# Kernel tuning notes

Hardware: AMD Instinct MI355X
Metric: run time of the kernel (lower is better)

The kernel has to match this reference:

```python
import jax, jax.numpy as jnp
import numpy as np

TAU = 2.0
BN_EPS = 1e-5
SG_ALPHA = 4.0
ATTN_SCALE = 0.125
NUM_HEADS = 8
T, B, C, H, W = 2, 16, 256, 64, 64


@jax.custom_vjp
def heaviside(x):
    return (x >= 0.0).astype(x.dtype)

def _hv_fwd(x):
    return (x >= 0.0).astype(x.dtype), x

def _hv_bwd(x, g):
    s = jax.nn.sigmoid(SG_ALPHA * x)
    return (g * SG_ALPHA * s * (1.0 - s),)

heaviside.defvjp(_hv_fwd, _hv_bwd)


def lif(x_seq, v_th):
    # MultiStepLIFNode: v <- v + (x - v)/tau ; spike = H(v - v_th); hard reset to 0 (detached)
    def step(v, x):
        v = v + (x - v) / TAU
        s = heaviside(v - v_th)
        v = v * (1.0 - jax.lax.stop_gradient(s))
        return v, s
    _, spikes = jax.lax.scan(step, jnp.zeros_like(x_seq[0]), x_seq)
    return spikes


def bn1d(x, gamma, beta, mean, var):
    # eval-mode BatchNorm1d over channel axis 2 of [T,B,C,N]
    inv = (gamma / jnp.sqrt(var + BN_EPS)).reshape(1, 1, -1, 1)
    shift = (beta - mean * gamma / jnp.sqrt(var + BN_EPS)).reshape(1, 1, -1, 1)
    return x * inv + shift


def to_heads(t):
    # [T,B,C,N] -> [T,B,h,N,d]
    t_, b_, c_, n_ = t.shape
    d = c_ // NUM_HEADS
    return t.transpose(0, 1, 3, 2).reshape(t_, b_, n_, NUM_HEADS, d).transpose(0, 1, 3, 2, 4)


def setup_inputs() -> dict:
    key = jax.random.key(0)
    ks = jax.random.split(key, 24)
    w_scale = 0.06  # ~1/sqrt(C)
    inp = {
        'x': jax.random.normal(ks[0], (T, B, C, H, W), jnp.float32),
        'wq': jax.random.normal(ks[1], (C, C), jnp.float32) * w_scale,
        'wk': jax.random.normal(ks[2], (C, C), jnp.float32) * w_scale,
        'wv': jax.random.normal(ks[3], (C, C), jnp.float32) * w_scale,
        'wp': jax.random.normal(ks[4], (C, C), jnp.float32) * w_scale,
        'bp': jax.random.normal(ks[5], (C,), jnp.float32) * 0.1,
    }
    i = 6
    for p in ('q', 'k', 'v', 'p'):
        inp[p + '_gamma'] = jax.random.uniform(ks[i], (C,), jnp.float32, 0.5, 1.5); i += 1
        inp[p + '_beta'] = jax.random.normal(ks[i], (C,), jnp.float32) * 0.1; i += 1
        inp[p + '_mean'] = jax.random.normal(ks[i], (C,), jnp.float32) * 0.1; i += 1
        inp[p + '_var'] = jax.random.uniform(ks[i], (C,), jnp.float32, 0.5, 1.5); i += 1
    return inp


def reference(x, wq, wk, wv, wp, bp,
              q_gamma, q_beta, q_mean, q_var,
              k_gamma, k_beta, k_mean, k_var,
              v_gamma, v_beta, v_mean, v_var,
              p_gamma, p_beta, p_mean, p_var):
    t_, b_, c_, h_, w_ = x.shape
    n_ = h_ * w_
    xs = lif(x, 1.0).reshape(t_, b_, c_, n_)  # proj_lif then flatten(3)
    # 1x1 conv == channel matmul, then BN, then LIF (binary spikes)
    q_out = lif(bn1d(jnp.einsum('oc,tbcn->tbon', wq, xs), q_gamma, q_beta, q_mean, q_var), 1.0)
    k_out = lif(bn1d(jnp.einsum('oc,tbcn->tbon', wk, xs), k_gamma, k_beta, k_mean, k_var), 1.0)
    v_out = lif(bn1d(jnp.einsum('oc,tbcn->tbon', wv, xs), v_gamma, v_beta, v_mean, v_var), 1.0)
    q = to_heads(q_out)
    k = to_heads(k_out)
    v = to_heads(v_out)
    # linear attention: (k^T @ v) then q @ (k^T v)
    kv = jnp.einsum('tbhnd,tbhne->tbhde', k, v)  # [T,B,h,d,d]
    attn = jnp.einsum('tbhnd,tbhde->tbhne', q, kv) * ATTN_SCALE
    attn = attn.transpose(0, 1, 2, 4, 3).reshape(t_, b_, c_, n_)
    s = lif(attn, 0.5)  # attn_lif with v_threshold=0.5
    out = jnp.einsum('oc,tbcn->tbon', wp, s) + bp.reshape(1, 1, -1, 1)
    out = bn1d(out, p_gamma, p_beta, p_mean, p_var).reshape(t_, b_, c_, h_, w_)
    return (out, xs, q_out, k_out, v_out)
```

## Files before the change

kernel.cpp:

```cpp
#include <hip/hip_runtime.h>
#include <cstdint>
#include <cstddef>

typedef __attribute__((ext_vector_type(8))) short short8;
typedef __attribute__((ext_vector_type(4))) float floatx4;
typedef __attribute__((ext_vector_type(4))) unsigned int uintx4;

#define DEV static __device__ __forceinline__

constexpr int NT = 2, NB = 16, NC = 256, NN = 4096, NHD = 8;
constexpr size_t NE1 = (size_t)NT * NB * NC * NN;
constexpr size_t TSTRIDE = (size_t)NB * NC * NN;

DEV unsigned short f2bf(float x) {
  unsigned int u = __builtin_bit_cast(unsigned int, x);
  unsigned int lsb = (u >> 16) & 1u;
  u += 0x7FFFu + lsb;
  return (unsigned short)(u >> 16);
}
DEV float bfb2f(unsigned short h) {
  unsigned int u = ((unsigned int)h) << 16;
  return __builtin_bit_cast(float, u);
}
DEV unsigned int pk2(unsigned short a, unsigned short b) {
  return (unsigned int)a | ((unsigned int)b << 16);
}
DEV int swz(int fr, int kk) { return fr * 4 + (kk ^ ((fr >> 1) & 3)); }
typedef __attribute__((address_space(3))) unsigned int lds_u32;
typedef __attribute__((address_space(1))) const unsigned int glb_u32;
DEV void gld_lds16(const void* g, void* l) {
  __builtin_amdgcn_global_load_lds((glb_u32*)g, (lds_u32*)l, 16, 0, 0);
}

__global__ __launch_bounds__(256) void prep_kernel(
    const float* __restrict__ wq, const float* __restrict__ wk, const float* __restrict__ wv,
    const float* __restrict__ wp, const float* __restrict__ bp,
    const float* __restrict__ qg, const float* __restrict__ qb, const float* __restrict__ qm, const float* __restrict__ qva,
    const float* __restrict__ kg, const float* __restrict__ kb, const float* __restrict__ km, const float* __restrict__ kva,
    const float* __restrict__ vg, const float* __restrict__ vb, const float* __restrict__ vm, const float* __restrict__ vva,
    const float* __restrict__ pg, const float* __restrict__ pb, const float* __restrict__ pm, const float* __restrict__ pva,
    unsigned short* __restrict__ Wqkv, unsigned short* __restrict__ Wp,
    float* __restrict__ invqkv, float* __restrict__ shqkv,
    float* __restrict__ invp, float* __restrict__ shp)
{
  int idx = blockIdx.x * 256 + threadIdx.x;
  if (idx < 196608) {
    int o = idx >> 8, c = idx & 255;
    const float* src = (o < 256) ? wq : (o < 512) ? wk : wv;
    float w = src[(size_t)(o & 255) * 256 + c];
    unsigned short h0 = f2bf(w);  float f0 = bfb2f(h0);
    float r1 = w - f0;
    unsigned short h1 = f2bf(r1); float f1 = bfb2f(h1);
    float r2 = r1 - f1;
    unsigned short h2 = f2bf(r2);
    Wqkv[idx] = h0; Wqkv[196608 + idx] = h1; Wqkv[393216 + idx] = h2;
  } else if (idx < 262144) {
    int j = idx - 196608;
    float w = wp[j];
    unsigned short h0 = f2bf(w);  float f0 = bfb2f(h0);
    float r1 = w - f0;
    unsigned short h1 = f2bf(r1); float f1 = bfb2f(h1);
    float r2 = r1 - f1;
    unsigned short h2 = f2bf(r2);
    Wp[j] = h0; Wp[65536 + j] = h1; Wp[131072 + j] = h2;
  } else if (idx < 262912) {
    int i = idx - 262144;
    int p = i >> 8, c = i & 255;
    float g  = (p == 0) ? qg[c] : (p == 1) ? kg[c] : vg[c];
    float be = (p == 0) ? qb[c] : (p == 1) ? kb[c] : vb[c];
    float mn = (p == 0) ? qm[c] : (p == 1) ? km[c] : vm[c];
    float vr = (p == 0) ? qva[c] : (p == 1) ? kva[c] : vva[c];
    float sq = sqrtf(vr + 1e-5f);
    invqkv[i] = g / sq;
    shqkv[i]  = be - (mn * g) / sq;
  } else if (idx < 263168) {
    int c = idx - 262912;
    float sq = sqrtf(pva[c] + 1e-5f);
    float iv = pg[c] / sq;
    invp[c] = iv;
    shp[c]  = pb[c] - (pm[c] * pg[c]) / sq + bp[c] * iv;
  }
}

__global__ __launch_bounds__(256) void lifx_kernel(const float* __restrict__ x,
                                                   float* __restrict__ xs_out,
                                                   unsigned short* __restrict__ xb16)
{
  __shared__ float tile[2][64][65];
  const int nt = blockIdx.x, ct = blockIdx.y, b = blockIdx.z;
  const int tid = threadIdx.x;
  const int ci = tid >> 2, cq = tid & 3;
  const int n0 = nt * 64, c0 = ct * 64;
  const size_t rowbase = ((size_t)(b * NC + c0 + ci)) * NN + n0 + cq * 16;
  const float* px0 = x + rowbase;
  const float* px1 = x + rowbase + TSTRIDE;
  float* po0 = xs_out + rowbase;
  float* po1 = xs_out + rowbase + TSTRIDE;
  #pragma unroll
  for (int jj = 0; jj < 4; jj++) {
    floatx4 x0 = *(const floatx4*)(px0 + jj * 4);
    floatx4 x1 = *(const floatx4*)(px1 + jj * 4);
    floatx4 s0v, s1v;
    #pragma unroll
    for (int e = 0; e < 4; e++) {
      float v1 = x0[e] * 0.5f;
      float s0 = (v1 >= 1.0f) ? 1.0f : 0.0f;
      float vr = v1 * (1.0f - s0);
      float v2 = vr + (x1[e] - vr) * 0.5f;
      float s1 = (v2 >= 1.0f) ? 1.0f : 0.0f;
      s0v[e] = s0; s1v[e] = s1;
      tile[0][ci][cq * 16 + jj * 4 + e] = s0;
      tile[1][ci][cq * 16 + jj * 4 + e] = s1;
    }
    *(floatx4*)(po0 + jj * 4) = s0v;
    *(floatx4*)(po1 + jj * 4) = s1v;
  }
  __syncthreads();
  const int ni = tid >> 2, cg = tid & 3;
  #pragma unroll
  for (int t = 0; t < 2; t++) {
    unsigned int wbits = 0;
    #pragma unroll
    for (int j = 0; j < 16; j++)
      wbits |= (tile[t][cg * 16 + j][ni] != 0.f ? 1u : 0u) << j;
    xb16[((size_t)((t * NB + b) * NN) + n0 + ni) * 16 + (c0 >> 4) + cg] = (unsigned short)wbits;
  }
}

__global__ __launch_bounds__(256, 3) void qkv_gemm(
    const unsigned short* __restrict__ xb16,
    const unsigned short* __restrict__ Wsp,
    const float* __restrict__ invv, const float* __restrict__ shv,
    float* __restrict__ dq, float* __restrict__ dk, float* __restrict__ dv,
    unsigned short* __restrict__ qbits, unsigned short* __restrict__ kbits,
    unsigned short* __restrict__ vbits)
{
  __shared__ __align__(16) unsigned char smem[33280];
  unsigned short* Al = (unsigned short*)smem;
  unsigned short* Bl = (unsigned short*)(smem + 24576);
  float* yl = (float*)smem;
  const int nt = blockIdx.x, mt = blockIdx.y, b = blockIdx.z;
  const int tid = threadIdx.x;
  const int lane = tid & 63, quad = lane >> 4, l16 = lane & 15;
  const int wave = tid >> 6;
  const int tw = wave >> 1, wm = (wave & 1) * 64;
  floatx4 acc[4][4] = {};
  const int bt = tid >> 7, brow = (tid >> 1) & 63, bhalf = tid & 1;
  const unsigned short* xrow = xb16 + ((size_t)((bt * NB + b) * NN) + nt * 64 + brow) * 16 + bhalf;

  for (int k0 = 0; k0 < 256; k0 += 32) {
    __syncthreads();
    #pragma unroll
    for (int j = 0; j < 6; j++) {
      int ci = j * 256 + tid;
      int fr = ci >> 2;
      int kk = (ci & 3) ^ ((fr >> 1) & 3);
      int s = fr >> 7, row = fr & 127;
      const unsigned short* g = Wsp + (size_t)s * 196608 + (size_t)(mt * 128 + row) * 256 + k0 + kk * 8;
      gld_lds16(g, Al + (size_t)ci * 8);
    }
    {
      unsigned int wb = xrow[k0 >> 4];
      uintx4 c0v, c1v;
      #pragma unroll
      for (int p = 0; p < 4; p++) {
        c0v[p] = pk2(((wb >> (2 * p)) & 1) ? 0x3F80 : 0, ((wb >> (2 * p + 1)) & 1) ? 0x3F80 : 0);
        c1v[p] = pk2(((wb >> (8 + 2 * p)) & 1) ? 0x3F80 : 0, ((wb >> (9 + 2 * p)) & 1) ? 0x3F80 : 0);
      }
      int fr = bt * 64 + brow;
      *(uintx4*)(Bl + (size_t)swz(fr, bhalf * 2)     * 8) = c0v;
      *(uintx4*)(Bl + (size_t)swz(fr, bhalf * 2 + 1) * 8) = c1v;
    }
    __syncthreads();

    short8 bfr[4];
    #pragma unroll
    for (int ni = 0; ni < 4; ni++) {
      int fr = tw * 64 + ni * 16 + l16;
      bfr[ni] = *(const short8*)(Bl + (size_t)swz(fr, quad) * 8);
    }
    #pragma unroll
    for (int mi = 0; mi < 4; mi++) {
      const int r0 = wm + mi * 16 + l16;
      short8 a0 = *(const short8*)(Al + (size_t)swz(      r0, quad) * 8);
      short8 a1 = *(const short8*)(Al + (size_t)swz(128 + r0, quad) * 8);
      short8 a2 = *(const short8*)(Al + (size_t)swz(256 + r0, quad) * 8);
      #pragma unroll
      for (int ni = 0; ni < 4; ni++) {
        acc[mi][ni] = __builtin_amdgcn_mfma_f32_16x16x32_bf16(a0, bfr[ni], acc[mi][ni], 0, 0, 0);
        acc[mi][ni] = __builtin_amdgcn_mfma_f32_16x16x32_bf16(a1, bfr[ni], acc[mi][ni], 0, 0, 0);
        acc[mi][ni] = __builtin_amdgcn_mfma_f32_16x16x32_bf16(a2, bfr[ni], acc[mi][ni], 0, 0, 0);
      }
    }
  }
  __syncthreads();
  if (tw == 0) {
    #pragma unroll
    for (int mi = 0; mi < 4; mi++)
      #pragma unroll
      for (int r = 0; r < 4; r++)
        #pragma unroll
        for (int ni = 0; ni < 4; ni++)
          yl[(size_t)(wm + mi * 16 + quad * 4 + r) * 65 + ni * 16 + l16] = acc[mi][ni][r];
  }
  __syncthreads();
  if (tw == 1) {
    #pragma unroll
    for (int mi = 0; mi < 4; mi++) {
      #pragma unroll
      for (int r = 0; r < 4; r++) {
        const int lrow = wm + mi * 16 + quad * 4 + r;
        const int orow = mt * 128 + lrow;
        const float iv = invv[orow], sh = shv[orow];
        const int widx = orow >> 8, c = orow & 255;
        float* dst = (widx == 0) ? dq : (widx == 1) ? dk : dv;
        unsigned short* bb = (widx == 0) ? qbits : (widx == 1) ? kbits : vbits;
        #pragma unroll
        for (int ni = 0; ni < 4; ni++) {
          const int n = nt * 64 + ni * 16 + l16;
          float y0 = yl[(size_t)lrow * 65 + ni * 16 + l16] * iv + sh;
          float y1 = acc[mi][ni][r] * iv + sh;
          float v1 = y0 * 0.5f;
          float s0 = (v1 >= 1.0f) ? 1.0f : 0.0f;
          float vr = v1 * (1.0f - s0);
          float v2 = vr + (y1 - vr) * 0.5f;
          float s1 = (v2 >= 1.0f) ? 1.0f : 0.0f;
          dst[(size_t)(b * NC + c) * NN + n] = s0;
          dst[(size_t)((NB + b) * NC + c) * NN + n] = s1;
          unsigned long long bl0 = __ballot(s0 != 0.0f);
          unsigned long long bl1 = __ballot(s1 != 0.0f);
          if (l16 == 0) {
            const int w16 = nt * 4 + ni;
            bb[(size_t)b        * 65536 + (size_t)c * 256 + w16] = (unsigned short)(bl0 >> (quad * 16));
            bb[(size_t)(NB + b) * 65536 + (size_t)c * 256 + w16] = (unsigned short)(bl1 >> (quad * 16));
          }
        }
      }
    }
  }
}

__global__ __launch_bounds__(256) void kv_kernel(const unsigned long long* __restrict__ kb,
                                                 const unsigned long long* __restrict__ vb,
                                                 float* __restrict__ kvout)
{
  __shared__ unsigned long long Kl[32 * 65];
  __shared__ unsigned long long Vl[32 * 65];
  const int h = blockIdx.x, z = blockIdx.y;
  const int tid = threadIdx.x;
  for (int i = tid; i < 2048; i += 256) {
    int row = i >> 6, w = i & 63;
    size_t g = (size_t)z * 16384 + (size_t)(h * 32 + row) * 64 + w;
    Kl[row * 65 + w] = kb[g];
    Vl[row * 65 + w] = vb[g];
  }
  __syncthreads();
  const int d = tid & 31, e0 = tid >> 5;
  int acc0 = 0, acc1 = 0, acc2 = 0, acc3 = 0;
  for (int w = 0; w < 64; w++) {
    unsigned long long ku = Kl[d * 65 + w];
    acc0 += __popcll(ku & Vl[(e0     ) * 65 + w]);
    acc1 += __popcll(ku & Vl[(e0 +  8) * 65 + w]);
    acc2 += __popcll(ku & Vl[(e0 + 16) * 65 + w]);
    acc3 += __popcll(ku & Vl[(e0 + 24) * 65 + w]);
  }
  float* o = kvout + ((size_t)(z * NHD + h) << 10);
  o[d * 32 + e0     ] = (float)acc0;
  o[d * 32 + e0 +  8] = (float)acc1;
  o[d * 32 + e0 + 16] = (float)acc2;
  o[d * 32 + e0 + 24] = (float)acc3;
}

__global__ __launch_bounds__(256) void attn_kernel(const unsigned short* __restrict__ qb16,
                                                   const float* __restrict__ kvout,
                                                   unsigned short* __restrict__ sb16)
{
  __shared__ float kvl[2][32][33];
  __shared__ unsigned short qt[2][32][16];
  const int nb = blockIdx.x, h = blockIdx.y, b = blockIdx.z;
  const int tid = threadIdx.x;
  const int wave = tid >> 6, lane = tid & 63, quad = lane >> 4, l16 = lane & 15;
  for (int i = tid; i < 2048; i += 256) {
    int t = i >> 10, j = i & 1023;
    kvl[t][j >> 5][j & 31] = kvout[((size_t)((t * NB + b) * NHD + h) << 10) + j];
  }
  for (int i = tid; i < 1024; i += 256) {
    int t = i >> 9, j = i & 511, row = j >> 4, w = j & 15;
    qt[t][row][w] = qb16[(size_t)(t * NB + b) * 65536 + (size_t)(h * 32 + row) * 256 + nb * 16 + w];
  }
  __syncthreads();
  short8 bf[2][2][2];
  #pragma unroll
  for (int t = 0; t < 2; t++) {
    #pragma unroll
    for (int eh = 0; eh < 2; eh++) {
      short8 bh, bl;
      #pragma unroll
      for (int j = 0; j < 8; j++) {
        float v = kvl[t][quad * 8 + j][eh * 16 + l16];
        unsigned short h0 = f2bf(v);
        float lo = v - bfb2f(h0);
        bh[j] = (short)h0;
        bl[j] = (short)f2bf(lo);
      }
      bf[t][0][eh] = bh; bf[t][1][eh] = bl;
    }
  }
  floatx4 acc[2][4][2] = {};
  #pragma unroll
  for (int t = 0; t < 2; t++) {
    #pragma unroll
    for (int nt = 0; nt < 4; nt++) {
      const int wv = wave * 4 + nt;
      short8 af;
      #pragma unroll
      for (int j = 0; j < 8; j++) {
        unsigned short w = qt[t][quad * 8 + j][wv];
        af[j] = (short)(((w >> l16) & 1) ? 0x3F80 : 0);
      }
      #pragma unroll
      for (int eh = 0; eh < 2; eh++) {
        acc[t][nt][eh] = __builtin_amdgcn_mfma_f32_16x16x32_bf16(af, bf[t][0][eh], acc[t][nt][eh], 0, 0, 0);
        acc[t][nt][eh] = __builtin_amdgcn_mfma_f32_16x16x32_bf16(af, bf[t][1][eh], acc[t][nt][eh], 0, 0, 0);
      }
    }
  }
  const int n0 = nb * 256 + wave * 64;
  #pragma unroll
  for (int nt = 0; nt < 4; nt++) {
    #pragma unroll
    for (int r = 0; r < 4; r++) {
      const int n = n0 + nt * 16 + quad * 4 + r;
      #pragma unroll
      for (int eh = 0; eh < 2; eh++) {
        float a0 = acc[0][nt][eh][r] * 0.125f;
        float a1 = acc[1][nt][eh][r] * 0.125f;
        float v1 = a0 * 0.5f;
        float s0 = (v1 >= 0.5f) ? 1.f : 0.f;
        float vr = v1 * (1.f - s0);
        float v2 = vr + (a1 - vr) * 0.5f;
        float s1 = (v2 >= 0.5f) ? 1.f : 0.f;
        unsigned long long bl0 = __ballot(s0 != 0.f);
        unsigned long long bl1 = __ballot(s1 != 0.f);
        if (l16 == 0) {
          const int w16 = h * 2 + eh;
          sb16[(size_t)b        * 65536 + (size_t)n * 16 + w16] = (unsigned short)(bl0 >> (quad * 16));
          sb16[(size_t)(NB + b) * 65536 + (size_t)n * 16 + w16] = (unsigned short)(bl1 >> (quad * 16));
        }
      }
    }
  }
}

__global__ __launch_bounds__(256, 3) void p_gemm(
    const unsigned short* __restrict__ sb16,
    const unsigned short* __restrict__ Wsp,
    const float* __restrict__ invv, const float* __restrict__ shv,
    float* __restrict__ dout)
{
  __shared__ __align__(16) unsigned char smem[32768];
  unsigned short* Al = (unsigned short*)smem;
  unsigned short* Bl = (unsigned short*)(smem + 24576);
  const int nt = blockIdx.x, mt = blockIdx.y, z = blockIdx.z;
  const int tid = threadIdx.x;
  const int lane = tid & 63, quad = lane >> 4, l16 = lane & 15;
  const int wave = tid >> 6;
  const int wm = (wave & 1) * 64, wn = (wave >> 1) * 64;
  floatx4 acc[4][4] = {};
  const int brow = tid & 127, bhalf = tid >> 7;

  for (int k0 = 0; k0 < 256; k0 += 32) {
    __syncthreads();
    #pragma unroll
    for (int j = 0; j < 6; j++) {
      int ci = j * 256 + tid;
      int fr = ci >> 2;
      int kk = (ci & 3) ^ ((fr >> 1) & 3);
      int s = fr >> 7, row = fr & 127;
      const unsigned short* g = Wsp + (size_t)s * 65536 + (size_t)(mt * 128 + row) * 256 + k0 + kk * 8;
      gld_lds16(g, Al + (size_t)ci * 8);
    }
    {
      unsigned short wb = sb16[(size_t)z * 65536 + (size_t)(nt * 128 + brow) * 16 + (k0 >> 4) + bhalf];
      uintx4 lo4, hi4;
      #pragma unroll
      for (int p = 0; p < 4; p++) {
        lo4[p] = pk2(((wb >> (2 * p)) & 1) ? 0x3F80 : 0, ((wb >> (2 * p + 1)) & 1) ? 0x3F80 : 0);
        hi4[p] = pk2(((wb >> (8 + 2 * p)) & 1) ? 0x3F80 : 0, ((wb >> (9 + 2 * p)) & 1) ? 0x3F80 : 0);
      }
      *(uintx4*)(Bl + (size_t)swz(brow, bhalf * 2)     * 8) = lo4;
      *(uintx4*)(Bl + (size_t)swz(brow, bhalf * 2 + 1) * 8) = hi4;
    }
    __syncthreads();

    short8 bfr[4];
    #pragma unroll
    for (int ni = 0; ni < 4; ni++) {
      int fr = wn + ni * 16 + l16;
      bfr[ni] = *(const short8*)(Bl + (size_t)swz(fr, quad) * 8);
    }
    #pragma unroll
    for (int mi = 0; mi < 4; mi++) {
      const int r0 = wm + mi * 16 + l16;
      short8 a0 = *(const short8*)(Al + (size_t)swz(      r0, quad) * 8);
      short8 a1 = *(const short8*)(Al + (size_t)swz(128 + r0, quad) * 8);
      short8 a2 = *(const short8*)(Al + (size_t)swz(256 + r0, quad) * 8);
      #pragma unroll
      for (int ni = 0; ni < 4; ni++) {
        acc[mi][ni] = __builtin_amdgcn_mfma_f32_16x16x32_bf16(a0, bfr[ni], acc[mi][ni], 0, 0, 0);
        acc[mi][ni] = __builtin_amdgcn_mfma_f32_16x16x32_bf16(a1, bfr[ni], acc[mi][ni], 0, 0, 0);
        acc[mi][ni] = __builtin_amdgcn_mfma_f32_16x16x32_bf16(a2, bfr[ni], acc[mi][ni], 0, 0, 0);
      }
    }
  }
  #pragma unroll
  for (int mi = 0; mi < 4; mi++) {
    #pragma unroll
    for (int r = 0; r < 4; r++) {
      const int orow = mt * 128 + wm + mi * 16 + quad * 4 + r;
      const float iv = invv[orow], sh = shv[orow];
      #pragma unroll
      for (int ni = 0; ni < 4; ni++) {
        const int n = nt * 128 + wn + ni * 16 + l16;
        dout[((size_t)(z * NC + orow)) * NN + n] = acc[mi][ni][r] * iv + sh;
      }
    }
  }
}

extern "C" void kernel_launch(void* const* d_in, const int* in_sizes, int n_in,
                              void* d_out, int out_size, void* d_ws, size_t ws_size,
                              hipStream_t stream) {
  (void)in_sizes; (void)n_in; (void)out_size; (void)ws_size;
  const float* x  = (const float*)d_in[0];
  const float* wq = (const float*)d_in[1];
  const float* wk = (const float*)d_in[2];
  const float* wv = (const float*)d_in[3];
  const float* wp = (const float*)d_in[4];
  const float* bp = (const float*)d_in[5];
  const float* qg = (const float*)d_in[6],  *qb = (const float*)d_in[7];
  const float* qm = (const float*)d_in[8],  *qva = (const float*)d_in[9];
  const float* kg = (const float*)d_in[10], *kb = (const float*)d_in[11];
  const float* km = (const float*)d_in[12], *kva = (const float*)d_in[13];
  const float* vg = (const float*)d_in[14], *vb = (const float*)d_in[15];
  const float* vm = (const float*)d_in[16], *vva = (const float*)d_in[17];
  const float* pg = (const float*)d_in[18], *pb = (const float*)d_in[19];
  const float* pm = (const float*)d_in[20], *pva = (const float*)d_in[21];

  float* out = (float*)d_out;
  float* xs  = out + NE1;
  float* dq  = out + 2 * NE1;
  float* dk  = out + 3 * NE1;
  float* dv  = out + 4 * NE1;

  char* ws = (char*)d_ws;
  unsigned short* xbits = (unsigned short*)ws;
  unsigned short* Wqkv  = (unsigned short*)(ws + 4194304);
  unsigned short* Wp    = (unsigned short*)(ws + 5373952);
  float* kvout          = (float*)(ws + 5767168);
  unsigned short* qbits = (unsigned short*)(ws + 6815744);
  unsigned short* kbits = (unsigned short*)(ws + 11010048);
  unsigned short* vbits = (unsigned short*)(ws + 15204352);
  unsigned short* sbits = (unsigned short*)(ws + 19398656);
  float* invqkv         = (float*)(ws + 23592960);
  float* shqkv          = invqkv + 768;
  float* invp           = shqkv + 768;
  float* shp            = invp + 256;

  prep_kernel<<<1028, 256, 0, stream>>>(wq, wk, wv, wp, bp,
                                        qg, qb, qm, qva, kg, kb, km, kva,
                                        vg, vb, vm, vva, pg, pb, pm, pva,
                                        Wqkv, Wp, invqkv, shqkv, invp, shp);
  lifx_kernel<<<dim3(64, 4, 16), 256, 0, stream>>>(x, xs, xbits);
  qkv_gemm<<<dim3(64, 6, 16), 256, 0, stream>>>(xbits, Wqkv, invqkv, shqkv,
                                                dq, dk, dv, qbits, kbits, vbits);
  kv_kernel<<<dim3(8, 32), 256, 0, stream>>>((const unsigned long long*)kbits,
                                             (const unsigned long long*)vbits, kvout);
  attn_kernel<<<dim3(16, 8, 16), 256, 0, stream>>>(qbits, kvout, sbits);
  p_gemm<<<dim3(32, 2, 32), 256, 0, stream>>>(sbits, Wp, invp, shp, out);
}
```

Measured before the change: 974.5 us.

## Drop LDS staging in spike GEMMs; build B fragments via bpermute, read weights directly

```diff
diff --git a/kernel.cpp b/kernel.cpp
--- a/kernel.cpp
+++ b/kernel.cpp
@@ -25,11 +25,12 @@
 DEV unsigned int pk2(unsigned short a, unsigned short b) {
   return (unsigned int)a | ((unsigned int)b << 16);
 }
-DEV int swz(int fr, int kk) { return fr * 4 + (kk ^ ((fr >> 1) & 3)); }
-typedef __attribute__((address_space(3))) unsigned int lds_u32;
-typedef __attribute__((address_space(1))) const unsigned int glb_u32;
-DEV void gld_lds16(const void* g, void* l) {
-  __builtin_amdgcn_global_load_lds((glb_u32*)g, (lds_u32*)l, 16, 0, 0);
+DEV short8 bits2frag(unsigned int w, int quad) {
+  short8 f;
+  #pragma unroll
+  for (int j = 0; j < 8; j++)
+    f[j] = (short)(((w >> (quad * 8 + j)) & 1) ? 0x3F80 : 0);
+  return f;
 }
 
 __global__ __launch_bounds__(256) void prep_kernel(
@@ -128,63 +129,45 @@
 }
 
 __global__ __launch_bounds__(256, 3) void qkv_gemm(
-    const unsigned short* __restrict__ xb16,
+    const unsigned int* __restrict__ xb32,
     const unsigned short* __restrict__ Wsp,
     const float* __restrict__ invv, const float* __restrict__ shv,
     float* __restrict__ dq, float* __restrict__ dk, float* __restrict__ dv,
     unsigned short* __restrict__ qbits, unsigned short* __restrict__ kbits,
     unsigned short* __restrict__ vbits)
 {
-  __shared__ __align__(16) unsigned char smem[33280];
-  unsigned short* Al = (unsigned short*)smem;
-  unsigned short* Bl = (unsigned short*)(smem + 24576);
-  float* yl = (float*)smem;
+  __shared__ float yl[128 * 65];
   const int nt = blockIdx.x, mt = blockIdx.y, b = blockIdx.z;
   const int tid = threadIdx.x;
   const int lane = tid & 63, quad = lane >> 4, l16 = lane & 15;
   const int wave = tid >> 6;
   const int tw = wave >> 1, wm = (wave & 1) * 64;
   floatx4 acc[4][4] = {};
-  const int bt = tid >> 7, brow = (tid >> 1) & 63, bhalf = tid & 1;
-  const unsigned short* xrow = xb16 + ((size_t)((bt * NB + b) * NN) + nt * 64 + brow) * 16 + bhalf;
-
-  for (int k0 = 0; k0 < 256; k0 += 32) {
-    __syncthreads();
-    #pragma unroll
-    for (int j = 0; j < 6; j++) {
-      int ci = j * 256 + tid;
-      int fr = ci >> 2;
-      int kk = (ci & 3) ^ ((fr >> 1) & 3);
-      int s = fr >> 7, row = fr & 127;
-      const unsigned short* g = Wsp + (size_t)s * 196608 + (size_t)(mt * 128 + row) * 256 + k0 + kk * 8;
-      gld_lds16(g, Al + (size_t)ci * 8);
-    }
-    {
-      unsigned int wb = xrow[k0 >> 4];
-      uintx4 c0v, c1v;
-      #pragma unroll
-      for (int p = 0; p < 4; p++) {
-        c0v[p] = pk2(((wb >> (2 * p)) & 1) ? 0x3F80 : 0, ((wb >> (2 * p + 1)) & 1) ? 0x3F80 : 0);
-        c1v[p] = pk2(((wb >> (8 + 2 * p)) & 1) ? 0x3F80 : 0, ((wb >> (9 + 2 * p)) & 1) ? 0x3F80 : 0);
-      }
-      int fr = bt * 64 + brow;
-      *(uintx4*)(Bl + (size_t)swz(fr, bhalf * 2)     * 8) = c0v;
-      *(uintx4*)(Bl + (size_t)swz(fr, bhalf * 2 + 1) * 8) = c1v;
-    }
-    __syncthreads();
-
+  const unsigned int* xr = xb32 + ((size_t)((tw * NB + b) * NN) + nt * 64 + lane) * 8;
+  uintx4 xw0 = *(const uintx4*)xr;
+  uintx4 xw1 = *(const uintx4*)(xr + 4);
+  int voff[12];
+  #pragma unroll
+  for (int s = 0; s < 3; s++)
+    #pragma unroll
+    for (int mi = 0; mi < 4; mi++)
+      voff[s * 4 + mi] = s * 196608 + (mt * 128 + wm + mi * 16 + l16) * 256 + quad * 8;
+
+  #pragma unroll
+  for (int kc = 0; kc < 8; kc++) {
+    unsigned int myw = (kc < 4) ? ((const unsigned int*)&xw0)[kc] : ((const unsigned int*)&xw1)[kc - 4];
     short8 bfr[4];
     #pragma unroll
     for (int ni = 0; ni < 4; ni++) {
-      int fr = tw * 64 + ni * 16 + l16;
-      bfr[ni] = *(const short8*)(Bl + (size_t)swz(fr, quad) * 8);
-    }
+      unsigned int src = (unsigned int)__builtin_amdgcn_ds_bpermute((ni * 16 + l16) * 4, (int)myw);
+      bfr[ni] = bits2frag(src, quad);
+    }
+    const unsigned short* gk = Wsp + kc * 32;
     #pragma unroll
     for (int mi = 0; mi < 4; mi++) {
-      const int r0 = wm + mi * 16 + l16;
-      short8 a0 = *(const short8*)(Al + (size_t)swz(      r0, quad) * 8);
-      short8 a1 = *(const short8*)(Al + (size_t)swz(128 + r0, quad) * 8);
-      short8 a2 = *(const short8*)(Al + (size_t)swz(256 + r0, quad) * 8);
+      short8 a0 = *(const short8*)(gk + voff[mi]);
+      short8 a1 = *(const short8*)(gk + voff[4 + mi]);
+      short8 a2 = *(const short8*)(gk + voff[8 + mi]);
       #pragma unroll
       for (int ni = 0; ni < 4; ni++) {
         acc[mi][ni] = __builtin_amdgcn_mfma_f32_16x16x32_bf16(a0, bfr[ni], acc[mi][ni], 0, 0, 0);
@@ -242,7 +225,8 @@
 
 __global__ __launch_bounds__(256) void kv_kernel(const unsigned long long* __restrict__ kb,
                                                  const unsigned long long* __restrict__ vb,
-                                                 float* __restrict__ kvout)
+                                                 unsigned short* __restrict__ kvhiT,
+                                                 unsigned short* __restrict__ kvloT)
 {
   __shared__ unsigned long long Kl[32 * 65];
   __shared__ unsigned long long Vl[32 * 65];
@@ -264,48 +248,44 @@
     acc2 += __popcll(ku & Vl[(e0 + 16) * 65 + w]);
     acc3 += __popcll(ku & Vl[(e0 + 24) * 65 + w]);
   }
-  float* o = kvout + ((size_t)(z * NHD + h) << 10);
-  o[d * 32 + e0     ] = (float)acc0;
-  o[d * 32 + e0 +  8] = (float)acc1;
-  o[d * 32 + e0 + 16] = (float)acc2;
-  o[d * 32 + e0 + 24] = (float)acc3;
+  unsigned short* oh = kvhiT + ((size_t)(z * NHD + h) << 10);
+  unsigned short* ol = kvloT + ((size_t)(z * NHD + h) << 10);
+  int accs[4] = {acc0, acc1, acc2, acc3};
+  #pragma unroll
+  for (int p = 0; p < 4; p++) {
+    float v = (float)accs[p];
+    unsigned short hi = f2bf(v);
+    float lo = v - bfb2f(hi);
+    oh[(e0 + 8 * p) * 32 + d] = hi;
+    ol[(e0 + 8 * p) * 32 + d] = f2bf(lo);
+  }
 }
 
 __global__ __launch_bounds__(256) void attn_kernel(const unsigned short* __restrict__ qb16,
-                                                   const float* __restrict__ kvout,
+                                                   const unsigned short* __restrict__ kvhiT,
+                                                   const unsigned short* __restrict__ kvloT,
                                                    unsigned short* __restrict__ sb16)
 {
-  __shared__ float kvl[2][32][33];
   __shared__ unsigned short qt[2][32][16];
   const int nb = blockIdx.x, h = blockIdx.y, b = blockIdx.z;
   const int tid = threadIdx.x;
   const int wave = tid >> 6, lane = tid & 63, quad = lane >> 4, l16 = lane & 15;
-  for (int i = tid; i < 2048; i += 256) {
-    int t = i >> 10, j = i & 1023;
-    kvl[t][j >> 5][j & 31] = kvout[((size_t)((t * NB + b) * NHD + h) << 10) + j];
-  }
   for (int i = tid; i < 1024; i += 256) {
     int t = i >> 9, j = i & 511, row = j >> 4, w = j & 15;
     qt[t][row][w] = qb16[(size_t)(t * NB + b) * 65536 + (size_t)(h * 32 + row) * 256 + nb * 16 + w];
   }
+  short8 bf[2][2][2];
+  #pragma unroll
+  for (int t = 0; t < 2; t++) {
+    const unsigned short* kh = kvhiT + ((size_t)((t * NB + b) * NHD + h) << 10);
+    const unsigned short* kl = kvloT + ((size_t)((t * NB + b) * NHD + h) << 10);
+    #pragma unroll
+    for (int eh = 0; eh < 2; eh++) {
+      bf[t][0][eh] = *(const short8*)(kh + (eh * 16 + l16) * 32 + quad * 8);
+      bf[t][1][eh] = *(const short8*)(kl + (eh * 16 + l16) * 32 + quad * 8);
+    }
+  }
   __syncthreads();
-  short8 bf[2][2][2];
-  #pragma unroll
-  for (int t = 0; t < 2; t++) {
-    #pragma unroll
-    for (int eh = 0; eh < 2; eh++) {
-      short8 bh, bl;
-      #pragma unroll
-      for (int j = 0; j < 8; j++) {
-        float v = kvl[t][quad * 8 + j][eh * 16 + l16];
-        unsigned short h0 = f2bf(v);
-        float lo = v - bfb2f(h0);
-        bh[j] = (short)h0;
-        bl[j] = (short)f2bf(lo);
-      }
-      bf[t][0][eh] = bh; bf[t][1][eh] = bl;
-    }
-  }
   floatx4 acc[2][4][2] = {};
   #pragma unroll
   for (int t = 0; t < 2; t++) {
@@ -353,58 +333,42 @@
 }
 
 __global__ __launch_bounds__(256, 3) void p_gemm(
-    const unsigned short* __restrict__ sb16,
+    const unsigned int* __restrict__ sb32,
     const unsigned short* __restrict__ Wsp,
     const float* __restrict__ invv, const float* __restrict__ shv,
     float* __restrict__ dout)
 {
-  __shared__ __align__(16) unsigned char smem[32768];
-  unsigned short* Al = (unsigned short*)smem;
-  unsigned short* Bl = (unsigned short*)(smem + 24576);
   const int nt = blockIdx.x, mt = blockIdx.y, z = blockIdx.z;
   const int tid = threadIdx.x;
   const int lane = tid & 63, quad = lane >> 4, l16 = lane & 15;
   const int wave = tid >> 6;
   const int wm = (wave & 1) * 64, wn = (wave >> 1) * 64;
   floatx4 acc[4][4] = {};
-  const int brow = tid & 127, bhalf = tid >> 7;
-
-  for (int k0 = 0; k0 < 256; k0 += 32) {
-    __syncthreads();
-    #pragma unroll
-    for (int j = 0; j < 6; j++) {
-      int ci = j * 256 + tid;
-      int fr = ci >> 2;
-      int kk = (ci & 3) ^ ((fr >> 1) & 3);
-      int s = fr >> 7, row = fr & 127;
-      const unsigned short* g = Wsp + (size_t)s * 65536 + (size_t)(mt * 128 + row) * 256 + k0 + kk * 8;
-      gld_lds16(g, Al + (size_t)ci * 8);
-    }
-    {
-      unsigned short wb = sb16[(size_t)z * 65536 + (size_t)(nt * 128 + brow) * 16 + (k0 >> 4) + bhalf];
-      uintx4 lo4, hi4;
-      #pragma unroll
-      for (int p = 0; p < 4; p++) {
-        lo4[p] = pk2(((wb >> (2 * p)) & 1) ? 0x3F80 : 0, ((wb >> (2 * p + 1)) & 1) ? 0x3F80 : 0);
-        hi4[p] = pk2(((wb >> (8 + 2 * p)) & 1) ? 0x3F80 : 0, ((wb >> (9 + 2 * p)) & 1) ? 0x3F80 : 0);
-      }
-      *(uintx4*)(Bl + (size_t)swz(brow, bhalf * 2)     * 8) = lo4;
-      *(uintx4*)(Bl + (size_t)swz(brow, bhalf * 2 + 1) * 8) = hi4;
-    }
-    __syncthreads();
-
+  const unsigned int* sr = sb32 + ((size_t)(z * NN) + nt * 128 + wn + lane) * 8;
+  uintx4 sw0 = *(const uintx4*)sr;
+  uintx4 sw1 = *(const uintx4*)(sr + 4);
+  int voff[12];
+  #pragma unroll
+  for (int s = 0; s < 3; s++)
+    #pragma unroll
+    for (int mi = 0; mi < 4; mi++)
+      voff[s * 4 + mi] = s * 65536 + (mt * 128 + wm + mi * 16 + l16) * 256 + quad * 8;
+
+  #pragma unroll
+  for (int kc = 0; kc < 8; kc++) {
+    unsigned int myw = (kc < 4) ? ((const unsigned int*)&sw0)[kc] : ((const unsigned int*)&sw1)[kc - 4];
     short8 bfr[4];
     #pragma unroll
     for (int ni = 0; ni < 4; ni++) {
-      int fr = wn + ni * 16 + l16;
-      bfr[ni] = *(const short8*)(Bl + (size_t)swz(fr, quad) * 8);
-    }
+      unsigned int src = (unsigned int)__builtin_amdgcn_ds_bpermute((ni * 16 + l16) * 4, (int)myw);
+      bfr[ni] = bits2frag(src, quad);
+    }
+    const unsigned short* gk = Wsp + kc * 32;
     #pragma unroll
     for (int mi = 0; mi < 4; mi++) {
-      const int r0 = wm + mi * 16 + l16;
-      short8 a0 = *(const short8*)(Al + (size_t)swz(      r0, quad) * 8);
-      short8 a1 = *(const short8*)(Al + (size_t)swz(128 + r0, quad) * 8);
-      short8 a2 = *(const short8*)(Al + (size_t)swz(256 + r0, quad) * 8);
+      short8 a0 = *(const short8*)(gk + voff[mi]);
+      short8 a1 = *(const short8*)(gk + voff[4 + mi]);
+      short8 a2 = *(const short8*)(gk + voff[8 + mi]);
       #pragma unroll
       for (int ni = 0; ni < 4; ni++) {
         acc[mi][ni] = __builtin_amdgcn_mfma_f32_16x16x32_bf16(a0, bfr[ni], acc[mi][ni], 0, 0, 0);
@@ -457,11 +421,12 @@
   unsigned short* xbits = (unsigned short*)ws;
   unsigned short* Wqkv  = (unsigned short*)(ws + 4194304);
   unsigned short* Wp    = (unsigned short*)(ws + 5373952);
-  float* kvout          = (float*)(ws + 5767168);
-  unsigned short* qbits = (unsigned short*)(ws + 6815744);
-  unsigned short* kbits = (unsigned short*)(ws + 11010048);
-  unsigned short* vbits = (unsigned short*)(ws + 15204352);
-  unsigned short* sbits = (unsigned short*)(ws + 19398656);
+  unsigned short* qbits = (unsigned short*)(ws + 5767168);
+  unsigned short* kbits = (unsigned short*)(ws + 9961472);
+  unsigned short* vbits = (unsigned short*)(ws + 14155776);
+  unsigned short* sbits = (unsigned short*)(ws + 18350080);
+  unsigned short* kvhiT = (unsigned short*)(ws + 22544384);
+  unsigned short* kvloT = (unsigned short*)(ws + 23068672);
   float* invqkv         = (float*)(ws + 23592960);
   float* shqkv          = invqkv + 768;
   float* invp           = shqkv + 768;
@@ -472,10 +437,13 @@
                                         vg, vb, vm, vva, pg, pb, pm, pva,
                                         Wqkv, Wp, invqkv, shqkv, invp, shp);
   lifx_kernel<<<dim3(64, 4, 16), 256, 0, stream>>>(x, xs, xbits);
-  qkv_gemm<<<dim3(64, 6, 16), 256, 0, stream>>>(xbits, Wqkv, invqkv, shqkv,
-                                                dq, dk, dv, qbits, kbits, vbits);
+  qkv_gemm<<<dim3(64, 6, 16), 256, 0, stream>>>((const unsigned int*)xbits, Wqkv,
+                                                invqkv, shqkv, dq, dk, dv,
+                                                qbits, kbits, vbits);
   kv_kernel<<<dim3(8, 32), 256, 0, stream>>>((const unsigned long long*)kbits,
-                                             (const unsigned long long*)vbits, kvout);
-  attn_kernel<<<dim3(16, 8, 16), 256, 0, stream>>>(qbits, kvout, sbits);
-  p_gemm<<<dim3(32, 2, 32), 256, 0, stream>>>(sbits, Wp, invp, shp, out);
-}
+                                             (const unsigned long long*)vbits,
+                                             kvhiT, kvloT);
+  attn_kernel<<<dim3(16, 8, 16), 256, 0, stream>>>(qbits, kvhiT, kvloT, sbits);
+  p_gemm<<<dim3(32, 2, 32), 256, 0, stream>>>((const unsigned int*)sbits, Wp,
+                                              invp, shp, out);
+}
```

Measured after the change: 1.176 ms. 20.6% more time.
